# Kernel optimization log

Hardware: AMD Instinct MI355X
Metric: run time of the kernel (lower is better)

The kernel has to match this reference:

```python
import jax, jax.numpy as jnp
import numpy as np
import math

B, S, D, H = 2, 2048, 2048, 16
HD = D // H  # 128


def setup_inputs() -> dict:
    key = jax.random.key(0)
    ks = jax.random.split(key, 6)
    x = jax.random.normal(ks[0], (B, S, D), dtype=jnp.float32)
    scale = 1.0 / math.sqrt(D)
    wq = jax.random.normal(ks[1], (D, D), dtype=jnp.float32) * scale
    wk = jax.random.normal(ks[2], (D, D), dtype=jnp.float32) * scale
    wv = jax.random.normal(ks[3], (D, D), dtype=jnp.float32) * scale
    wo = jax.random.normal(ks[4], (D, D), dtype=jnp.float32) * scale
    # rotary frequencies: freqs_cis[t, j] = exp(i * t / theta^(2j/HD))
    theta = 10000.0
    inv = 1.0 / (theta ** (jnp.arange(0, HD, 2, dtype=jnp.float32) / HD))  # [HD//2]
    ang = jnp.arange(S, dtype=jnp.float32)[:, None] * inv[None, :]  # [S, HD//2]
    freqs_cos = jnp.cos(ang)
    freqs_sin = jnp.sin(ang)
    # causal additive mask
    mask = jnp.where(jnp.tril(jnp.ones((S, S), dtype=bool)), 0.0, -1e9)
    mask = mask[None, None, :, :].astype(jnp.float32)
    return {"x": x, "wq": wq, "wk": wk, "wv": wv, "wo": wo,
            "freqs_cos": freqs_cos, "freqs_sin": freqs_sin, "mask": mask}


def _rope(t, cos, sin):
    # t: [B, S, H, HD]; cos/sin: [S, HD//2]
    b, s, h, d = t.shape
    t2 = t.reshape(b, s, h, d // 2, 2)
    re, im = t2[..., 0], t2[..., 1]
    c = cos[None, :, None, :]
    sn = sin[None, :, None, :]
    out_re = re * c - im * sn
    out_im = re * sn + im * c
    return jnp.stack([out_re, out_im], axis=-1).reshape(b, s, h, d)


def reference(x, wq, wk, wv, wo, freqs_cos, freqs_sin, mask):
    b, s, _ = x.shape
    xq = (x @ wq.T).reshape(b, s, H, HD)
    xk = (x @ wk.T).reshape(b, s, H, HD)
    xv = (x @ wv.T).reshape(b, s, H, HD)
    xq = _rope(xq, freqs_cos, freqs_sin)
    xk = _rope(xk, freqs_cos, freqs_sin)
    # [B, H, S, HD]
    q = xq.transpose(0, 2, 1, 3)
    k = xk.transpose(0, 2, 1, 3)
    v = xv.transpose(0, 2, 1, 3)
    scores = jnp.einsum("bhqd,bhkd->bhqk", q, k) / math.sqrt(HD)
    scores = scores + mask
    probs = jax.nn.softmax(scores.astype(jnp.float32), axis=-1).astype(q.dtype)
    out = jnp.einsum("bhqk,bhkd->bhqd", probs, v)
    out = out.transpose(0, 2, 1, 3).reshape(b, s, -1)
    return out @ wo.T
```

## Files before the change

kernel.cpp:

```cpp
#include <hip/hip_runtime.h>
#include <math.h>

#define BATCH 2
#define SEQ 2048
#define DMODEL 2048
#define NH 16
#define HD 128

typedef __bf16 bf16x8 __attribute__((ext_vector_type(8)));
typedef __bf16 bf16x4 __attribute__((ext_vector_type(4)));
typedef float f32x4 __attribute__((ext_vector_type(4)));
typedef float f32x16 __attribute__((ext_vector_type(16)));

#define GLL16(dst, src)                                                          \
  __builtin_amdgcn_global_load_lds(                                              \
      (const __attribute__((address_space(1))) void*)(src),                      \
      (__attribute__((address_space(3))) void*)(dst), 16, 0, 0)

__global__ __launch_bounds__(256) void split_fp32(const float* __restrict__ src,
                                                  __bf16* __restrict__ hi,
                                                  __bf16* __restrict__ lo) {
  const size_t i = (size_t)blockIdx.x * 256 + threadIdx.x;
  const float4 v = ((const float4*)src)[i];
  bf16x4 h, L;
  h[0] = (__bf16)v.x; h[1] = (__bf16)v.y; h[2] = (__bf16)v.z; h[3] = (__bf16)v.w;
  L[0] = (__bf16)(v.x - (float)h[0]);
  L[1] = (__bf16)(v.y - (float)h[1]);
  L[2] = (__bf16)(v.z - (float)h[2]);
  L[3] = (__bf16)(v.w - (float)h[3]);
  ((bf16x4*)hi)[i] = h;
  ((bf16x4*)lo)[i] = L;
}

template <int EMIT>
__global__ __launch_bounds__(512, 2) void gemm8(const __bf16* __restrict__ Ah,
                                                const __bf16* __restrict__ Al,
                                                const __bf16* __restrict__ Bh,
                                                const __bf16* __restrict__ Bl,
                                                void* __restrict__ Cout) {
  extern __shared__ char sm[];
  constexpr int NT = 96;
  const int tid = threadIdx.x;
  const int l = tid & 63, w = tid >> 6;
  const int lg = l >> 4, lm = l & 15;
  const int wr = w >> 1, wc = w & 1;

  const int bid = (int)blockIdx.x;
  const int X = bid & 7, sub = bid >> 3;
  const int mb = (X & 3) * 4 + (sub >> 3);
  const int nb = (X >> 2) * 8 + (sub & 7);
  const int m0 = mb * 256, n0 = nb * 128;

  const __bf16* segA[3] = {Ah, Al, Ah};
  const __bf16* segB[3] = {Bh, Bh, Bl};

  const int srow = l >> 3;
  const int co = ((l & 7) ^ srow) * 8;

  char* const Abuf = sm;
  char* const Bbuf = sm + 98304;

  auto stageB = [&](int tb) {
    char* bd = Bbuf + (tb & 1) * 16384;
    const __bf16* sb = segB[tb >> 5];
    const int kw = (tb & 31) * 64;
#pragma unroll
    for (int j = 0; j < 2; ++j)
      GLL16(bd + (w * 2 + j) * 1024,
            sb + (size_t)(n0 + (w * 2 + j) * 8 + srow) * 2048 + kw + co);
  };
  auto stageAu = [&](int ta, int slot, int u) {
    char* ad = Abuf + slot * 32768 + u * 16384;
    const __bf16* sa = segA[ta >> 5];
    const int kw = (ta & 31) * 64;
#pragma unroll
    for (int j = 0; j < 2; ++j)
      GLL16(ad + (w * 2 + j) * 1024,
            sa + (size_t)(m0 + u * 128 + (w * 2 + j) * 8 + srow) * 2048 + kw + co);
  };

  stageAu(0, 0, 0); stageAu(0, 0, 1);
  stageB(0);
  stageAu(1, 1, 0); stageAu(1, 1, 1);

  f32x4 acc[4][4];
#pragma unroll
  for (int i = 0; i < 4; ++i)
#pragma unroll
    for (int j = 0; j < 4; ++j) { f32x4 z = {0.f, 0.f, 0.f, 0.f}; acc[i][j] = z; }

  int sA = 0, sA2 = 2;
  const int swz = lm & 7;

  for (int t = 0; t < NT; ++t) {
    if (t + 1 < NT) { asm volatile("s_waitcnt vmcnt(4)" ::: "memory"); }
    else            { asm volatile("s_waitcnt vmcnt(0)" ::: "memory"); }
    __builtin_amdgcn_sched_barrier(0);
    __builtin_amdgcn_s_barrier();

    const char* Ab = Abuf + sA * 32768;
    const char* Bb = Bbuf + (t & 1) * 16384;

    bf16x8 b0[4], b1[4], a[2];

    if (t + 1 < NT) stageB(t + 1);
#pragma unroll
    for (int j = 0; j < 4; ++j)
      b0[j] = *(const bf16x8*)(Bb + (wc * 64 + j * 16 + lm) * 128 + ((lg ^ swz) << 4));
#pragma unroll
    for (int i = 0; i < 2; ++i)
      a[i] = *(const bf16x8*)(Ab + (wr * 64 + i * 16 + lm) * 128 + ((lg ^ swz) << 4));
    __builtin_amdgcn_s_barrier();
    __builtin_amdgcn_s_setprio(1);
#pragma unroll
    for (int i = 0; i < 2; ++i)
#pragma unroll
      for (int j = 0; j < 4; ++j)
        acc[i][j] = __builtin_amdgcn_mfma_f32_16x16x32_bf16(a[i], b0[j], acc[i][j], 0, 0, 0);
    __builtin_amdgcn_s_setprio(0);

    if (t + 2 < NT) stageAu(t + 2, sA2, 0);
#pragma unroll
    for (int j = 0; j < 4; ++j)
      b1[j] = *(const bf16x8*)(Bb + (wc * 64 + j * 16 + lm) * 128 + (((4 + lg) ^ swz) << 4));
#pragma unroll
    for (int i = 0; i < 2; ++i)
      a[i] = *(const bf16x8*)(Ab + (wr * 64 + i * 16 + lm) * 128 + (((4 + lg) ^ swz) << 4));
    __builtin_amdgcn_s_barrier();
    __builtin_amdgcn_s_setprio(1);
#pragma unroll
    for (int i = 0; i < 2; ++i)
#pragma unroll
      for (int j = 0; j < 4; ++j)
        acc[i][j] = __builtin_amdgcn_mfma_f32_16x16x32_bf16(a[i], b1[j], acc[i][j], 0, 0, 0);
    __builtin_amdgcn_s_setprio(0);

    if (t + 2 < NT) stageAu(t + 2, sA2, 1);
#pragma unroll
    for (int i = 0; i < 2; ++i)
      a[i] = *(const bf16x8*)(Ab + (wr * 64 + (2 + i) * 16 + lm) * 128 + ((lg ^ swz) << 4));
    __builtin_amdgcn_s_barrier();
    __builtin_amdgcn_s_setprio(1);
#pragma unroll
    for (int i = 0; i < 2; ++i)
#pragma unroll
      for (int j = 0; j < 4; ++j)
        acc[2 + i][j] = __builtin_amdgcn_mfma_f32_16x16x32_bf16(a[i], b0[j], acc[2 + i][j], 0, 0, 0);
    __builtin_amdgcn_s_setprio(0);

#pragma unroll
    for (int i = 0; i < 2; ++i)
      a[i] = *(const bf16x8*)(Ab + (wr * 64 + (2 + i) * 16 + lm) * 128 + (((4 + lg) ^ swz) << 4));
    __builtin_amdgcn_s_barrier();
    __builtin_amdgcn_s_setprio(1);
#pragma unroll
    for (int i = 0; i < 2; ++i)
#pragma unroll
      for (int j = 0; j < 4; ++j)
        acc[2 + i][j] = __builtin_amdgcn_mfma_f32_16x16x32_bf16(a[i], b1[j], acc[2 + i][j], 0, 0, 0);
    __builtin_amdgcn_s_setprio(0);

    sA = (sA == 2) ? 0 : sA + 1;
    sA2 = (sA2 == 2) ? 0 : sA2 + 1;
  }

#pragma unroll
  for (int i = 0; i < 4; ++i)
#pragma unroll
    for (int j = 0; j < 4; ++j)
#pragma unroll
      for (int r = 0; r < 4; ++r) {
        const size_t row = (size_t)(m0 + wr * 64 + i * 16 + lg * 4 + r);
        const size_t col = (size_t)(n0 + wc * 64 + j * 16 + lm);
        if (EMIT == 0) ((float*)Cout)[row * 2048 + col] = acc[i][j][r];
        else           ((__bf16*)Cout)[row * 2048 + col] = (__bf16)acc[i][j][r];
      }
}

__global__ __launch_bounds__(256) void rope_bf16(__bf16* __restrict__ t,
                                                 const float* __restrict__ cosp,
                                                 const float* __restrict__ sinp,
                                                 float scale) {
  const size_t i4 = (size_t)blockIdx.x * 256 + threadIdx.x;
  const size_t e = i4 * 4;
  const int srow = (int)((e >> 11) & 2047);
  const int p = (int)(e & 127) >> 1;
  bf16x4 vv = *(bf16x4*)(t + e);
  const float c0 = cosp[srow * 64 + p],     s0 = sinp[srow * 64 + p];
  const float c1 = cosp[srow * 64 + p + 1], s1 = sinp[srow * 64 + p + 1];
  const float re0 = (float)vv[0], im0 = (float)vv[1];
  const float re1 = (float)vv[2], im1 = (float)vv[3];
  bf16x4 o;
  o[0] = (__bf16)((re0 * c0 - im0 * s0) * scale);
  o[1] = (__bf16)((re0 * s0 + im0 * c0) * scale);
  o[2] = (__bf16)((re1 * c1 - im1 * s1) * scale);
  o[3] = (__bf16)((re1 * s1 + im1 * c1) * scale);
  *(bf16x4*)(t + e) = o;
}

static __device__ __forceinline__ unsigned pk2(float a, float b) {
  unsigned short x = __builtin_bit_cast(unsigned short, (__bf16)a);
  unsigned short y = __builtin_bit_cast(unsigned short, (__bf16)b);
  return ((unsigned)y << 16) | (unsigned)x;
}

__global__ __launch_bounds__(256) void attn_mfma2(const __bf16* __restrict__ q,
                                                  const __bf16* __restrict__ k,
                                                  const __bf16* __restrict__ v,
                                                  __bf16* __restrict__ oh,
                                                  __bf16* __restrict__ ol) {
  __shared__ __align__(16) char Ks[64 * 272];
  __shared__ __align__(16) char Vt[128 * 144];

  const int tid = threadIdx.x;
  const int l = tid & 63, w = tid >> 6;
  const int l31 = l & 31, hg = l >> 5;

  const int f = (int)blockIdx.x;
  const int X = f & 7, t = f >> 3;
  const int g = X * 4 + (t & 3);
  const int qt = 15 - (t >> 2);
  const int b = g >> 4, h = g & 15;
  const int q0 = qt * 128;
  const size_t bh = (size_t)b * SEQ * DMODEL + (size_t)h * HD;

  bf16x8 qf[8];
  {
    const __bf16* qr = q + bh + (size_t)(q0 + 32 * w + l31) * DMODEL;
#pragma unroll
    for (int ks = 0; ks < 8; ++ks) qf[ks] = *(const bf16x8*)(qr + ks * 16 + hg * 8);
  }

  f32x16 accO[4];
#pragma unroll
  for (int dt = 0; dt < 4; ++dt)
#pragma unroll
    for (int i = 0; i < 16; ++i) accO[dt][i] = 0.f;
  float m_own = -1e30f, l_own = 0.f;

  const int srT = tid >> 4;
  const int scT = tid & 15;
  const int nkt = 2 * qt + 2;
  const int qg_own = q0 + 32 * w + l31;
  const int qg_min = q0 + 32 * w;

  bf16x8 kst[4], vst[4];
#pragma unroll
  for (int rnd = 0; rnd < 4; ++rnd) {
    const int r = srT + 16 * rnd;
    const size_t ga = bh + (size_t)(r) * DMODEL + scT * 8;
    kst[rnd] = *(const bf16x8*)(k + ga);
    vst[rnd] = *(const bf16x8*)(v + ga);
  }

  for (int kt = 0; kt < nkt; ++kt) {
    const int k0 = kt * 64;
    __syncthreads();
#pragma unroll
    for (int rnd = 0; rnd < 4; ++rnd) {
      const int r = srT + 16 * rnd;
      *(bf16x8*)(Ks + r * 272 + ((scT * 16) ^ (((r >> 3) & 7) << 4))) = kst[rnd];
      const int swz = (scT & 7) << 4;
      const int cb = (2 * r) ^ swz;
#pragma unroll
      for (int e = 0; e < 8; ++e)
        *(__bf16*)(Vt + (scT * 8 + e) * 144 + cb) = vst[rnd][e];
    }
    __syncthreads();
    if (kt + 1 < nkt) {
#pragma unroll
      for (int rnd = 0; rnd < 4; ++rnd) {
        const int r = srT + 16 * rnd;
        const size_t ga = bh + (size_t)((kt + 1) * 64 + r) * DMODEL + scT * 8;
        kst[rnd] = *(const bf16x8*)(k + ga);
        vst[rnd] = *(const bf16x8*)(v + ga);
      }
    }
    if (k0 > qg_min + 31) continue;

    f32x16 sc[2];
#pragma unroll
    for (int mt = 0; mt < 2; ++mt)
#pragma unroll
      for (int i = 0; i < 16; ++i) sc[mt][i] = 0.f;
#pragma unroll
    for (int mt = 0; mt < 2; ++mt) {
      const int row = mt * 32 + l31;
      const char* kr = Ks + row * 272;
      const int sx = ((row >> 3) & 7) << 4;
#pragma unroll
      for (int ks = 0; ks < 8; ++ks) {
        bf16x8 kf = *(const bf16x8*)(kr + ((ks * 32 + hg * 16) ^ sx));
        sc[mt] = __builtin_amdgcn_mfma_f32_32x32x16_bf16(kf, qf[ks], sc[mt], 0, 0, 0);
      }
    }

    if (k0 + 63 > qg_min) {
#pragma unroll
      for (int mt = 0; mt < 2; ++mt)
#pragma unroll
        for (int ri = 0; ri < 16; ++ri) {
          const int kg = k0 + mt * 32 + (ri & 3) + 8 * (ri >> 2) + 4 * hg;
          if (kg > qg_own) sc[mt][ri] = -INFINITY;
        }
    }

    float tm = -INFINITY;
#pragma unroll
    for (int mt = 0; mt < 2; ++mt)
#pragma unroll
      for (int ri = 0; ri < 16; ++ri) tm = fmaxf(tm, sc[mt][ri]);
    tm = fmaxf(tm, __shfl_xor(tm, 32));

    if (__any(tm > m_own)) {
      const float mnew = fmaxf(m_own, tm);
      const float alpha = __expf(m_own - mnew);
      m_own = mnew;
      l_own *= alpha;
#pragma unroll
      for (int ri = 0; ri < 16; ++ri) {
        const float a = __shfl(alpha, (ri & 3) + 8 * (ri >> 2) + 4 * hg);
#pragma unroll
        for (int dt = 0; dt < 4; ++dt) accO[dt][ri] *= a;
      }
    }
    float rs = 0.f;
#pragma unroll
    for (int mt = 0; mt < 2; ++mt)
#pragma unroll
      for (int ri = 0; ri < 16; ++ri) {
        const float p = __expf(sc[mt][ri] - m_own);
        sc[mt][ri] = p;
        rs += p;
      }
    rs += __shfl_xor(rs, 32);
    l_own += rs;

#pragma unroll
    for (int kk = 0; kk < 4; ++kk) {
      const int mt = kk >> 1, J8 = (kk & 1) * 8;
      unsigned oL0 = pk2(sc[mt][J8 + 0], sc[mt][J8 + 1]);
      unsigned oL1 = pk2(sc[mt][J8 + 2], sc[mt][J8 + 3]);
      unsigned oH0 = pk2(sc[mt][J8 + 4], sc[mt][J8 + 5]);
      unsigned oH1 = pk2(sc[mt][J8 + 6], sc[mt][J8 + 7]);
      unsigned s0 = hg ? oL0 : oH0;
      unsigned s1 = hg ? oL1 : oH1;
      const unsigned r0 = (unsigned)__shfl_xor((int)s0, 32);
      const unsigned r1 = (unsigned)__shfl_xor((int)s1, 32);
      int4 fi;
      fi.x = (int)(hg ? r0 : oL0);
      fi.y = (int)(hg ? r1 : oL1);
      fi.z = (int)(hg ? oH0 : r0);
      fi.w = (int)(hg ? oH1 : r1);
      const bf16x8 pa = __builtin_bit_cast(bf16x8, fi);
      const int kb = (kk * 32 + hg * 16);
#pragma unroll
      for (int dt = 0; dt < 4; ++dt) {
        const int d = dt * 32 + l31;
        bf16x8 vf = *(const bf16x8*)(Vt + d * 144 + (kb ^ (((d >> 3) & 7) << 4)));
        accO[dt] = __builtin_amdgcn_mfma_f32_32x32x16_bf16(pa, vf, accO[dt], 0, 0, 0);
      }
    }
  }

  const float inv_own = 1.f / l_own;
#pragma unroll
  for (int ri = 0; ri < 16; ++ri) {
    const int row = (ri & 3) + 8 * (ri >> 2) + 4 * hg;
    const float il = __shfl(inv_own, row & 31);
    const size_t rbase = bh + (size_t)(q0 + 32 * w + row) * DMODEL;
#pragma unroll
    for (int dt = 0; dt < 4; ++dt) {
      const float val = accO[dt][ri] * il;
      const size_t idx = rbase + dt * 32 + l31;
      const __bf16 hv = (__bf16)val;
      oh[idx] = hv;
      ol[idx] = (__bf16)(val - (float)hv);
    }
  }
}

extern "C" void kernel_launch(void* const* d_in, const int* in_sizes, int n_in,
                              void* d_out, int out_size, void* d_ws, size_t ws_size,
                              hipStream_t stream) {
  const float* x  = (const float*)d_in[0];
  const float* wq = (const float*)d_in[1];
  const float* wk = (const float*)d_in[2];
  const float* wv = (const float*)d_in[3];
  const float* wo = (const float*)d_in[4];
  const float* fc = (const float*)d_in[5];
  const float* fs = (const float*)d_in[6];

  const size_t NTOK = (size_t)BATCH * SEQ;
  const size_t NE   = NTOK * DMODEL;

  char* wsb = (char*)d_ws;
  __bf16* xh = (__bf16*)wsb;
  __bf16* xl = xh + NE;
  __bf16* wh = (__bf16*)(wsb + 2 * NE * 2);
  __bf16* wl = wh + (size_t)DMODEL * DMODEL;
  __bf16* vb = (__bf16*)(wsb + 2 * NE * 2 + 2 * (size_t)DMODEL * DMODEL * 2);
  __bf16* oh = xh;
  __bf16* ol = xl;
  __bf16* qb = (__bf16*)d_out;
  __bf16* kb = qb + NE;

  const int sx = (int)(NE / 4 / 256);
  const int sw = DMODEL * DMODEL / 4 / 256;
  const int SMEM = 131072;

  (void)hipFuncSetAttribute((const void*)gemm8<1>,
                            hipFuncAttributeMaxDynamicSharedMemorySize, SMEM);
  (void)hipFuncSetAttribute((const void*)gemm8<0>,
                            hipFuncAttributeMaxDynamicSharedMemorySize, SMEM);

  split_fp32<<<sx, 256, 0, stream>>>(x, xh, xl);

  split_fp32<<<sw, 256, 0, stream>>>(wq, wh, wl);
  gemm8<1><<<256, 512, SMEM, stream>>>(xh, xl, wh, wl, qb);
  split_fp32<<<sw, 256, 0, stream>>>(wk, wh, wl);
  gemm8<1><<<256, 512, SMEM, stream>>>(xh, xl, wh, wl, kb);
  split_fp32<<<sw, 256, 0, stream>>>(wv, wh, wl);
  gemm8<1><<<256, 512, SMEM, stream>>>(xh, xl, wh, wl, vb);

  rope_bf16<<<sx, 256, 0, stream>>>(qb, fc, fs, 0.08838834764831845f);
  rope_bf16<<<sx, 256, 0, stream>>>(kb, fc, fs, 1.0f);

  attn_mfma2<<<dim3(512), 256, 0, stream>>>(qb, kb, vb, oh, ol);

  split_fp32<<<sw, 256, 0, stream>>>(wo, wh, wl);
  gemm8<0><<<256, 512, SMEM, stream>>>(oh, ol, wh, wl, (float*)d_out);
}
```

Measured before the change: 673.4 us.

## Restructure GEMM k-loop into two phases and merge RoPE launches

The GEMM inner loop goes from four barrier-separated MFMA phases with 2x4 tiles to two phases with 4x4 tiles. All A and B fragments for a k-half are loaded up front, and the async staging of the next tiles is issued before the compute. This halves the barriers per iteration, at the cost of more live registers and different load/compute overlap. The two RoPE launches for Q and K are also merged into one grid that uses blockIdx.y to select the tensor and scale, saving a kernel launch.

```diff
diff --git a/kernel.cpp b/kernel.cpp
--- a/kernel.cpp
+++ b/kernel.cpp
@@ -100,64 +100,39 @@
 
     const char* Ab = Abuf + sA * 32768;
     const char* Bb = Bbuf + (t & 1) * 16384;
-
-    bf16x8 b0[4], b1[4], a[2];
-
+    bf16x8 a[4], b[4];
+
+#pragma unroll
+    for (int j = 0; j < 4; ++j)
+      b[j] = *(const bf16x8*)(Bb + (wc * 64 + j * 16 + lm) * 128 + ((lg ^ swz) << 4));
+#pragma unroll
+    for (int i = 0; i < 4; ++i)
+      a[i] = *(const bf16x8*)(Ab + (wr * 64 + i * 16 + lm) * 128 + ((lg ^ swz) << 4));
     if (t + 1 < NT) stageB(t + 1);
-#pragma unroll
-    for (int j = 0; j < 4; ++j)
-      b0[j] = *(const bf16x8*)(Bb + (wc * 64 + j * 16 + lm) * 128 + ((lg ^ swz) << 4));
-#pragma unroll
-    for (int i = 0; i < 2; ++i)
-      a[i] = *(const bf16x8*)(Ab + (wr * 64 + i * 16 + lm) * 128 + ((lg ^ swz) << 4));
+    if (t + 2 < NT) stageAu(t + 2, sA2, 0);
     __builtin_amdgcn_s_barrier();
     __builtin_amdgcn_s_setprio(1);
 #pragma unroll
-    for (int i = 0; i < 2; ++i)
+    for (int i = 0; i < 4; ++i)
 #pragma unroll
       for (int j = 0; j < 4; ++j)
-        acc[i][j] = __builtin_amdgcn_mfma_f32_16x16x32_bf16(a[i], b0[j], acc[i][j], 0, 0, 0);
+        acc[i][j] = __builtin_amdgcn_mfma_f32_16x16x32_bf16(a[i], b[j], acc[i][j], 0, 0, 0);
     __builtin_amdgcn_s_setprio(0);
 
-    if (t + 2 < NT) stageAu(t + 2, sA2, 0);
 #pragma unroll
     for (int j = 0; j < 4; ++j)
-      b1[j] = *(const bf16x8*)(Bb + (wc * 64 + j * 16 + lm) * 128 + (((4 + lg) ^ swz) << 4));
-#pragma unroll
-    for (int i = 0; i < 2; ++i)
+      b[j] = *(const bf16x8*)(Bb + (wc * 64 + j * 16 + lm) * 128 + (((4 + lg) ^ swz) << 4));
+#pragma unroll
+    for (int i = 0; i < 4; ++i)
       a[i] = *(const bf16x8*)(Ab + (wr * 64 + i * 16 + lm) * 128 + (((4 + lg) ^ swz) << 4));
+    if (t + 2 < NT) stageAu(t + 2, sA2, 1);
     __builtin_amdgcn_s_barrier();
     __builtin_amdgcn_s_setprio(1);
 #pragma unroll
-    for (int i = 0; i < 2; ++i)
+    for (int i = 0; i < 4; ++i)
 #pragma unroll
       for (int j = 0; j < 4; ++j)
-        acc[i][j] = __builtin_amdgcn_mfma_f32_16x16x32_bf16(a[i], b1[j], acc[i][j], 0, 0, 0);
-    __builtin_amdgcn_s_setprio(0);
-
-    if (t + 2 < NT) stageAu(t + 2, sA2, 1);
-#pragma unroll
-    for (int i = 0; i < 2; ++i)
-      a[i] = *(const bf16x8*)(Ab + (wr * 64 + (2 + i) * 16 + lm) * 128 + ((lg ^ swz) << 4));
-    __builtin_amdgcn_s_barrier();
-    __builtin_amdgcn_s_setprio(1);
-#pragma unroll
-    for (int i = 0; i < 2; ++i)
-#pragma unroll
-      for (int j = 0; j < 4; ++j)
-        acc[2 + i][j] = __builtin_amdgcn_mfma_f32_16x16x32_bf16(a[i], b0[j], acc[2 + i][j], 0, 0, 0);
-    __builtin_amdgcn_s_setprio(0);
-
-#pragma unroll
-    for (int i = 0; i < 2; ++i)
-      a[i] = *(const bf16x8*)(Ab + (wr * 64 + (2 + i) * 16 + lm) * 128 + (((4 + lg) ^ swz) << 4));
-    __builtin_amdgcn_s_barrier();
-    __builtin_amdgcn_s_setprio(1);
-#pragma unroll
-    for (int i = 0; i < 2; ++i)
-#pragma unroll
-      for (int j = 0; j < 4; ++j)
-        acc[2 + i][j] = __builtin_amdgcn_mfma_f32_16x16x32_bf16(a[i], b1[j], acc[2 + i][j], 0, 0, 0);
+        acc[i][j] = __builtin_amdgcn_mfma_f32_16x16x32_bf16(a[i], b[j], acc[i][j], 0, 0, 0);
     __builtin_amdgcn_s_setprio(0);
 
     sA = (sA == 2) ? 0 : sA + 1;
@@ -177,10 +152,12 @@
       }
 }
 
-__global__ __launch_bounds__(256) void rope_bf16(__bf16* __restrict__ t,
+__global__ __launch_bounds__(256) void rope_bf16(__bf16* __restrict__ q,
+                                                 __bf16* __restrict__ k,
                                                  const float* __restrict__ cosp,
-                                                 const float* __restrict__ sinp,
-                                                 float scale) {
+                                                 const float* __restrict__ sinp) {
+  __bf16* t = blockIdx.y ? k : q;
+  const float scale = blockIdx.y ? 1.0f : 0.08838834764831845f;
   const size_t i4 = (size_t)blockIdx.x * 256 + threadIdx.x;
   const size_t e = i4 * 4;
   const int srow = (int)((e >> 11) & 2047);
@@ -423,8 +400,7 @@
   split_fp32<<<sw, 256, 0, stream>>>(wv, wh, wl);
   gemm8<1><<<256, 512, SMEM, stream>>>(xh, xl, wh, wl, vb);
 
-  rope_bf16<<<sx, 256, 0, stream>>>(qb, fc, fs, 0.08838834764831845f);
-  rope_bf16<<<sx, 256, 0, stream>>>(kb, fc, fs, 1.0f);
+  rope_bf16<<<dim3(sx, 2), 256, 0, stream>>>(qb, kb, fc, fs);
 
   attn_mfma2<<<dim3(512), 256, 0, stream>>>(qb, kb, vb, oh, ol);
 
```

Result: faster. 651.1 us (-3.3%).
